# Kernel optimization log

Hardware: AMD Instinct MI355X
Metric: run time of the kernel (lower is better)

The kernel has to match this reference:

```python
import jax, jax.numpy as jnp
import numpy as np

N = 100000      # nodes
K = 16          # sampled neighbors per node (aggregate_num)
D = 256         # features_dim
DO = 256        # out_feat_dim
ALPHA = 0.2     # LeakyReLU negative slope (args.alpha)
EPS = 1e-12     # F.normalize eps


def setup_inputs() -> dict:
    key = jax.random.key(0)
    k1, k2, k3 = jax.random.split(key, 3)
    h = jax.random.normal(k1, (N, D), dtype=jnp.float32)
    neighbors = jax.random.randint(k2, (N, K), 0, N, dtype=jnp.int64)
    # Xavier-uniform-ish init for W_gcn
    limit = float(np.sqrt(6.0 / (D + DO)))
    W_gcn = jax.random.uniform(k3, (D, DO), dtype=jnp.float32, minval=-limit, maxval=limit)
    return {"h": h, "neighbors": neighbors, "W_gcn": W_gcn}


def reference(h, neighbors, W_gcn):
    # GCN-style aggregate: mean of self feature and K sampled neighbor features.
    # (dropout on neighbor feats is identity in eval mode)
    neigh_sum = jnp.sum(h[neighbors], axis=1)          # [N, D] gather + reduce
    agg = (h + neigh_sum) / jnp.float32(K + 1)         # [N, D]
    z = agg @ W_gcn                                    # [N, DO]
    z = jnp.where(z >= 0, z, ALPHA * z)                # LeakyReLU
    norm = jnp.sqrt(jnp.sum(z * z, axis=1, keepdims=True))
    return z / jnp.maximum(norm, EPS)                  # L2 normalize per row
```

## Files before the change

kernel.cpp:

```cpp
#include <hip/hip_runtime.h>
#include <stdint.h>

#define N_NODES 100000
#define KNBR 16
#define ALPHA 0.2f

typedef __attribute__((ext_vector_type(8))) short bf16x8;
typedef __attribute__((ext_vector_type(4))) float f32x4;
typedef __attribute__((ext_vector_type(4))) unsigned int u32x4;
typedef unsigned short u16;
typedef unsigned int u32;
typedef unsigned char u8;

static __device__ __forceinline__ u16 f2bf(float f) {
  u32 u = __builtin_bit_cast(u32, f);
  u += 0x7fffu + ((u >> 16) & 1u);
  return (u16)(u >> 16);
}

__global__ __launch_bounds__(256) void prep_w_kernel(const float* __restrict__ W,
                                                     u16* __restrict__ Wb) {
  const int t = blockIdx.x * 256 + threadIdx.x;
  const int l = t & 63;
  const int ct = (t >> 6) & 15;
  const int ks = t >> 10;
  const int colbase = ct * 16 + (l & 15);
  const int k0 = ks * 32 + (l >> 4) * 8;
  u32 wq[4];
#pragma unroll
  for (int q = 0; q < 4; ++q) {
    const u16 b0 = f2bf(W[(k0 + 2 * q) * 256 + colbase]);
    const u16 b1 = f2bf(W[(k0 + 2 * q + 1) * 256 + colbase]);
    wq[q] = (u32)b0 | ((u32)b1 << 16);
  }
  uint4 o = {wq[0], wq[1], wq[2], wq[3]};
  *(uint4*)(Wb + (size_t)t * 8) = o;
}

__global__ __launch_bounds__(256, 4) void gemm_kernel(const float* __restrict__ h,
                                                      const u16* __restrict__ Wb,
                                                      u8* __restrict__ Yq,
                                                      float* __restrict__ scale) {
  __shared__ __align__(16) u16 aS[32 * 256];
  __shared__ float redS[4][32];
  __shared__ float invSS[32];
  const int tid = threadIdx.x;
  const int blk = blockIdx.x;
  const size_t base = (size_t)blk * (32 * 256);

#pragma unroll
  for (int i = 0; i < 8; ++i) {
    const int flat = i * 1024 + tid * 4;
    const int row = flat >> 8, d0 = flat & 255;
    const f32x4 v = __builtin_nontemporal_load((const f32x4*)(h + base + flat));
    uint2 o;
    o.x = (u32)f2bf(v[0]) | ((u32)f2bf(v[1]) << 16);
    o.y = (u32)f2bf(v[2]) | ((u32)f2bf(v[3]) << 16);
    *(uint2*)((char*)aS + row * 512 + ((d0 * 2) ^ ((row & 7) << 4))) = o;
  }
  __syncthreads();

  const int l = tid & 63, wv = tid >> 6;
  const int l15 = l & 15, lg = l >> 4;
  f32x4 acc[2][4] = {};
  const uint4* wbL = ((const uint4*)Wb) + (size_t)(wv * 4) * 64 + l;
  const char* aggB = (const char*)aS;
  const int rb0 = l15 * 512;
  const int xm = (l15 & 7) << 4;
#pragma unroll 2
  for (int ks = 0; ks < 8; ++ks) {
    const int offk = ((ks * 64) + lg * 16) ^ xm;
    const bf16x8 a0 = *(const bf16x8*)(aggB + rb0 + offk);
    const bf16x8 a1 = *(const bf16x8*)(aggB + rb0 + 8192 + offk);
#pragma unroll
    for (int c = 0; c < 4; ++c) {
      const uint4 bw = wbL[ks * 1024 + c * 64];
      const bf16x8 b = __builtin_bit_cast(bf16x8, bw);
      acc[0][c] = __builtin_amdgcn_mfma_f32_16x16x32_bf16(a0, b, acc[0][c], 0, 0, 0);
      acc[1][c] = __builtin_amdgcn_mfma_f32_16x16x32_bf16(a1, b, acc[1][c], 0, 0, 0);
    }
  }

#pragma unroll
  for (int rt = 0; rt < 2; ++rt)
#pragma unroll
    for (int j = 0; j < 4; ++j) {
      float m = 0.f;
#pragma unroll
      for (int c = 0; c < 4; ++c) m = fmaxf(m, fabsf(acc[rt][c][j]));
      m = fmaxf(m, __shfl_xor(m, 1)); m = fmaxf(m, __shfl_xor(m, 2));
      m = fmaxf(m, __shfl_xor(m, 4)); m = fmaxf(m, __shfl_xor(m, 8));
      redS[wv][rt * 16 + lg * 4 + j] = m;
    }
  __syncthreads();
  if (tid < 32) {
    float m = fmaxf(fmaxf(redS[0][tid], redS[1][tid]),
                    fmaxf(redS[2][tid], redS[3][tid]));
    m = fmaxf(m, 1e-20f);
    scale[blk * 32 + tid] = m * (1.0f / 127.0f);
    invSS[tid] = 127.0f / m;
  }
  __syncthreads();

  u8* qS = (u8*)aS;
#pragma unroll
  for (int rt = 0; rt < 2; ++rt)
#pragma unroll
    for (int j = 0; j < 4; ++j) {
      const int r = rt * 16 + lg * 4 + j;
      const float inv = invSS[r];
      const int sw = ((r >> 2) & 7) << 5;
#pragma unroll
      for (int c = 0; c < 4; ++c) {
        float q = rintf(acc[rt][c][j] * inv);
        q = fminf(127.f, fmaxf(-127.f, q));
        qS[r * 256 + ((wv * 64 + c * 16 + l15) ^ sw)] = (u8)((int)q + 128);
      }
    }
  __syncthreads();

  const u32x4* q4 = (const u32x4*)aS;
  u32x4* yg = (u32x4*)(Yq + (size_t)blk * 8192);
#pragma unroll
  for (int q = 0; q < 2; ++q) {
    const int f = q * 4096 + tid * 16;
    const int row = f >> 8, col = f & 255;
    const int colx = col ^ (((row >> 2) & 7) << 5);
    __builtin_nontemporal_store(q4[(row * 256 + colx) >> 4], &yg[f >> 4]);
  }
}

__global__ __launch_bounds__(256) void gather_kernel(const u8* __restrict__ Yq,
                                                     const float* __restrict__ scale,
                                                     const int* __restrict__ nbr,
                                                     float* __restrict__ out) {
  const int tid = threadIdx.x;
  const int lane = tid & 63, wv = tid >> 6;
  const int node = __builtin_amdgcn_readfirstlane(blockIdx.x * 4 + wv);

  int idx[17];
  idx[0] = node;
#pragma unroll
  for (int j = 0; j < 16; ++j) idx[j + 1] = nbr[node * KNBR + j];

  float s[17];
#pragma unroll
  for (int j = 0; j < 17; ++j) s[j] = scale[idx[j]];

  u32 v[17];
#pragma unroll
  for (int j = 0; j < 17; ++j)
    v[j] = *(const u32*)(Yq + (size_t)idx[j] * 256 + lane * 4);

  float a0 = 0.f, a1 = 0.f, a2 = 0.f, a3 = 0.f, S = 0.f;
#pragma unroll
  for (int j = 0; j < 17; ++j) {
    float f0, f1, f2, f3;
    asm("v_cvt_f32_ubyte0 %0, %1" : "=v"(f0) : "v"(v[j]));
    asm("v_cvt_f32_ubyte1 %0, %1" : "=v"(f1) : "v"(v[j]));
    asm("v_cvt_f32_ubyte2 %0, %1" : "=v"(f2) : "v"(v[j]));
    asm("v_cvt_f32_ubyte3 %0, %1" : "=v"(f3) : "v"(v[j]));
    S += s[j];
    a0 = fmaf(s[j], f0, a0);
    a1 = fmaf(s[j], f1, a1);
    a2 = fmaf(s[j], f2, a2);
    a3 = fmaf(s[j], f3, a3);
  }
  const float sc = 1.0f / 17.0f, bias = 128.0f * S;
  a0 = (a0 - bias) * sc; a1 = (a1 - bias) * sc;
  a2 = (a2 - bias) * sc; a3 = (a3 - bias) * sc;
  a0 = (a0 >= 0.f) ? a0 : ALPHA * a0;
  a1 = (a1 >= 0.f) ? a1 : ALPHA * a1;
  a2 = (a2 >= 0.f) ? a2 : ALPHA * a2;
  a3 = (a3 >= 0.f) ? a3 : ALPHA * a3;

  float ss = a0 * a0 + a1 * a1 + a2 * a2 + a3 * a3;
  ss += __shfl_xor(ss, 1);  ss += __shfl_xor(ss, 2);
  ss += __shfl_xor(ss, 4);  ss += __shfl_xor(ss, 8);
  ss += __shfl_xor(ss, 16); ss += __shfl_xor(ss, 32);
  const float inv = 1.0f / fmaxf(sqrtf(ss), 1e-12f);

  f32x4 o = {a0 * inv, a1 * inv, a2 * inv, a3 * inv};
  __builtin_nontemporal_store(o, (f32x4*)(out + (size_t)node * 256 + lane * 4));
}

extern "C" void kernel_launch(void* const* d_in, const int* in_sizes, int n_in,
                              void* d_out, int out_size, void* d_ws, size_t ws_size,
                              hipStream_t stream) {
  const float* h = (const float*)d_in[0];
  const int* nbr = (const int*)d_in[1];
  const float* W = (const float*)d_in[2];
  float* out = (float*)d_out;

  u16* Wb = (u16*)d_ws;
  float* scale = (float*)((char*)d_ws + (1 << 17));
  u8* Yq = (u8*)((char*)d_ws + (1 << 20));

  prep_w_kernel<<<32, 256, 0, stream>>>(W, Wb);
  gemm_kernel<<<N_NODES / 32, 256, 0, stream>>>(h, Wb, Yq, scale);
  gather_kernel<<<N_NODES / 4, 256, 0, stream>>>(Yq, scale, nbr, out);
}
```

Baseline: 113.4 us.

## Slice quantized features by column for cache-local gather, add separate norm pass

The GEMM output is stored as eight column slices of 32 bytes per node, so each slice (3.2 MB) can stay cache-resident while a slice-gather kernel sums neighbor rows for that slice. The slice kernel writes partial bf16 results and per-slice sums of squares, and a new norm kernel reduces them and writes the normalized fp32 output. This trades extra global traffic (bf16 intermediate plus a third kernel launch) and bf16 rounding of the output for better locality of the random gathers. The fallback gather kernel also now loads the neighbor indices and scales once per wave and broadcasts them with readlane.

```diff
diff --git a/kernel.cpp b/kernel.cpp
--- a/kernel.cpp
+++ b/kernel.cpp
@@ -4,10 +4,14 @@
 #define N_NODES 100000
 #define KNBR 16
 #define ALPHA 0.2f
+#define SDIM 32
+#define NSLICE 8
+#define ANODES 64
 
 typedef __attribute__((ext_vector_type(8))) short bf16x8;
 typedef __attribute__((ext_vector_type(4))) float f32x4;
 typedef __attribute__((ext_vector_type(4))) unsigned int u32x4;
+typedef __attribute__((ext_vector_type(2))) unsigned int u32x2;
 typedef unsigned short u16;
 typedef unsigned int u32;
 typedef unsigned char u8;
@@ -16,6 +20,9 @@
   u32 u = __builtin_bit_cast(u32, f);
   u += 0x7fffu + ((u >> 16) & 1u);
   return (u16)(u >> 16);
+}
+static __device__ __forceinline__ float bf2f(u16 s) {
+  return __builtin_bit_cast(float, ((u32)s) << 16);
 }
 
 __global__ __launch_bounds__(256) void prep_w_kernel(const float* __restrict__ W,
@@ -37,6 +44,7 @@
   *(uint4*)(Wb + (size_t)t * 8) = o;
 }
 
+template <bool SLICED>
 __global__ __launch_bounds__(256, 4) void gemm_kernel(const float* __restrict__ h,
                                                       const u16* __restrict__ Wb,
                                                       u8* __restrict__ Yq,
@@ -120,14 +128,123 @@
   __syncthreads();
 
   const u32x4* q4 = (const u32x4*)aS;
-  u32x4* yg = (u32x4*)(Yq + (size_t)blk * 8192);
-#pragma unroll
-  for (int q = 0; q < 2; ++q) {
-    const int f = q * 4096 + tid * 16;
-    const int row = f >> 8, col = f & 255;
-    const int colx = col ^ (((row >> 2) & 7) << 5);
-    __builtin_nontemporal_store(q4[(row * 256 + colx) >> 4], &yg[f >> 4]);
-  }
+  if (SLICED) {
+#pragma unroll
+    for (int rr = 0; rr < 2; ++rr) {
+      const int f = rr * 256 + tid;
+      const int s = f >> 6;
+      const int nodeL = (f >> 1) & 31;
+      const int half = f & 1;
+      const int colx = (s * 32 + half * 16) ^ (((nodeL >> 2) & 7) << 5);
+      const u32x4 piece = q4[(nodeL * 256 + colx) >> 4];
+      __builtin_nontemporal_store(
+          piece, (u32x4*)(Yq + (size_t)s * ((size_t)N_NODES * SDIM) +
+                          (size_t)(blk * 32 + nodeL) * SDIM + half * 16));
+    }
+  } else {
+    u32x4* yg = (u32x4*)(Yq + (size_t)blk * 8192);
+#pragma unroll
+    for (int q = 0; q < 2; ++q) {
+      const int f = q * 4096 + tid * 16;
+      const int row = f >> 8, col = f & 255;
+      const int colx = col ^ (((row >> 2) & 7) << 5);
+      __builtin_nontemporal_store(q4[(row * 256 + colx) >> 4], &yg[f >> 4]);
+    }
+  }
+}
+
+__global__ __launch_bounds__(256) void slice_gather_kernel(
+    const u8* __restrict__ Yq, const float* __restrict__ scale,
+    const int* __restrict__ nbr, u16* __restrict__ zws,
+    float* __restrict__ ssp) {
+  __shared__ int nbrS[ANODES * 17];
+  const int tid = threadIdx.x;
+  const int s = blockIdx.x & 7;
+  const int chunk = blockIdx.x >> 3;
+  const int nodeBase = chunk * ANODES;
+
+  {
+    const int n = tid >> 2, j4 = tid & 3;
+    int4 v = {0, 0, 0, 0};
+    if (nodeBase + n < N_NODES)
+      v = ((const int4*)(nbr + (size_t)nodeBase * KNBR))[tid];
+    nbrS[n * 17 + j4 * 4 + 0] = v.x;
+    nbrS[n * 17 + j4 * 4 + 1] = v.y;
+    nbrS[n * 17 + j4 * 4 + 2] = v.z;
+    nbrS[n * 17 + j4 * 4 + 3] = v.w;
+  }
+  __syncthreads();
+
+  const u8* Ys = Yq + (size_t)s * ((size_t)N_NODES * SDIM);
+  const int sub = tid & 7;
+
+#pragma unroll
+  for (int p = 0; p < 2; ++p) {
+    const int nl = p * 32 + (tid >> 3);
+    const int node = nodeBase + nl;
+    if (node < N_NODES) {
+      int idx[17];
+      idx[0] = node;
+#pragma unroll
+      for (int j = 0; j < 16; ++j) idx[j + 1] = nbrS[nl * 17 + j];
+
+      u32 v[17];
+#pragma unroll
+      for (int j = 0; j < 17; ++j)
+        v[j] = *(const u32*)(Ys + (size_t)idx[j] * SDIM + sub * 4);
+      float sj[17];
+#pragma unroll
+      for (int j = 0; j < 17; ++j) sj[j] = scale[idx[j]];
+
+      float a0 = 0.f, a1 = 0.f, a2 = 0.f, a3 = 0.f, S = 0.f;
+#pragma unroll
+      for (int j = 0; j < 17; ++j) {
+        float f0, f1, f2, f3;
+        asm("v_cvt_f32_ubyte0 %0, %1" : "=v"(f0) : "v"(v[j]));
+        asm("v_cvt_f32_ubyte1 %0, %1" : "=v"(f1) : "v"(v[j]));
+        asm("v_cvt_f32_ubyte2 %0, %1" : "=v"(f2) : "v"(v[j]));
+        asm("v_cvt_f32_ubyte3 %0, %1" : "=v"(f3) : "v"(v[j]));
+        S += sj[j];
+        a0 = fmaf(sj[j], f0, a0);
+        a1 = fmaf(sj[j], f1, a1);
+        a2 = fmaf(sj[j], f2, a2);
+        a3 = fmaf(sj[j], f3, a3);
+      }
+      const float sc = 1.0f / 17.0f, bias = 128.0f * S;
+      a0 = (a0 - bias) * sc; a1 = (a1 - bias) * sc;
+      a2 = (a2 - bias) * sc; a3 = (a3 - bias) * sc;
+      a0 = (a0 >= 0.f) ? a0 : ALPHA * a0;
+      a1 = (a1 >= 0.f) ? a1 : ALPHA * a1;
+      a2 = (a2 >= 0.f) ? a2 : ALPHA * a2;
+      a3 = (a3 >= 0.f) ? a3 : ALPHA * a3;
+
+      float ss = a0 * a0 + a1 * a1 + a2 * a2 + a3 * a3;
+      ss += __shfl_xor(ss, 1); ss += __shfl_xor(ss, 2); ss += __shfl_xor(ss, 4);
+
+      u32x2 o = {(u32)f2bf(a0) | ((u32)f2bf(a1) << 16),
+                 (u32)f2bf(a2) | ((u32)f2bf(a3) << 16)};
+      __builtin_nontemporal_store(
+          o, (u32x2*)(zws + (size_t)node * 256 + s * SDIM + sub * 4));
+      if (sub == 0) ssp[node * 8 + s] = ss;
+    }
+  }
+}
+
+__global__ __launch_bounds__(256) void norm_kernel(const u16* __restrict__ zws,
+                                                   const float* __restrict__ ssp,
+                                                   float* __restrict__ out) {
+  const int tid = threadIdx.x;
+  const int lane = tid & 63, wv = tid >> 6;
+  const int node = __builtin_amdgcn_readfirstlane(blockIdx.x * 4 + wv);
+
+  float f = ssp[node * 8 + (lane & 7)];
+  f += __shfl_xor(f, 1); f += __shfl_xor(f, 2); f += __shfl_xor(f, 4);
+  const float inv = 1.0f / fmaxf(sqrtf(f), 1e-12f);
+
+  const u32x2 z = *(const u32x2*)(zws + (size_t)node * 256 + lane * 4);
+  f32x4 o = {bf2f((u16)(z.x & 0xffff)) * inv, bf2f((u16)(z.x >> 16)) * inv,
+             bf2f((u16)(z.y & 0xffff)) * inv, bf2f((u16)(z.y >> 16)) * inv};
+  __builtin_nontemporal_store(o, (f32x4*)(out + (size_t)node * 256 + lane * 4));
 }
 
 __global__ __launch_bounds__(256) void gather_kernel(const u8* __restrict__ Yq,
@@ -138,33 +255,40 @@
   const int lane = tid & 63, wv = tid >> 6;
   const int node = __builtin_amdgcn_readfirstlane(blockIdx.x * 4 + wv);
 
-  int idx[17];
-  idx[0] = node;
-#pragma unroll
-  for (int j = 0; j < 16; ++j) idx[j + 1] = nbr[node * KNBR + j];
-
-  float s[17];
-#pragma unroll
-  for (int j = 0; j < 17; ++j) s[j] = scale[idx[j]];
+  const int il = nbr[node * KNBR + (lane & 15)];
+  const float vscale = scale[il];
+  const float sself = scale[node];
+  const u32* yb = (const u32*)Yq;
 
   u32 v[17];
-#pragma unroll
-  for (int j = 0; j < 17; ++j)
-    v[j] = *(const u32*)(Yq + (size_t)idx[j] * 256 + lane * 4);
-
-  float a0 = 0.f, a1 = 0.f, a2 = 0.f, a3 = 0.f, S = 0.f;
-#pragma unroll
-  for (int j = 0; j < 17; ++j) {
+  v[0] = yb[(size_t)node * 64 + lane];
+#pragma unroll
+  for (int j = 0; j < 16; ++j) {
+    const int r = __builtin_amdgcn_readlane(il, j);
+    v[j + 1] = yb[(size_t)r * 64 + lane];
+  }
+
+  float a0, a1, a2, a3, S = sself;
+  {
     float f0, f1, f2, f3;
-    asm("v_cvt_f32_ubyte0 %0, %1" : "=v"(f0) : "v"(v[j]));
-    asm("v_cvt_f32_ubyte1 %0, %1" : "=v"(f1) : "v"(v[j]));
-    asm("v_cvt_f32_ubyte2 %0, %1" : "=v"(f2) : "v"(v[j]));
-    asm("v_cvt_f32_ubyte3 %0, %1" : "=v"(f3) : "v"(v[j]));
-    S += s[j];
-    a0 = fmaf(s[j], f0, a0);
-    a1 = fmaf(s[j], f1, a1);
-    a2 = fmaf(s[j], f2, a2);
-    a3 = fmaf(s[j], f3, a3);
+    asm("v_cvt_f32_ubyte0 %0, %1" : "=v"(f0) : "v"(v[0]));
+    asm("v_cvt_f32_ubyte1 %0, %1" : "=v"(f1) : "v"(v[0]));
+    asm("v_cvt_f32_ubyte2 %0, %1" : "=v"(f2) : "v"(v[0]));
+    asm("v_cvt_f32_ubyte3 %0, %1" : "=v"(f3) : "v"(v[0]));
+    a0 = sself * f0; a1 = sself * f1; a2 = sself * f2; a3 = sself * f3;
+  }
+#pragma unroll
+  for (int j = 0; j < 16; ++j) {
+    const float s = __builtin_bit_cast(
+        float, __builtin_amdgcn_readlane(__builtin_bit_cast(int, vscale), j));
+    float f0, f1, f2, f3;
+    asm("v_cvt_f32_ubyte0 %0, %1" : "=v"(f0) : "v"(v[j + 1]));
+    asm("v_cvt_f32_ubyte1 %0, %1" : "=v"(f1) : "v"(v[j + 1]));
+    asm("v_cvt_f32_ubyte2 %0, %1" : "=v"(f2) : "v"(v[j + 1]));
+    asm("v_cvt_f32_ubyte3 %0, %1" : "=v"(f3) : "v"(v[j + 1]));
+    S += s;
+    a0 = fmaf(s, f0, a0); a1 = fmaf(s, f1, a1);
+    a2 = fmaf(s, f2, a2); a3 = fmaf(s, f3, a3);
   }
   const float sc = 1.0f / 17.0f, bias = 128.0f * S;
   a0 = (a0 - bias) * sc; a1 = (a1 - bias) * sc;
@@ -192,11 +316,24 @@
   const float* W = (const float*)d_in[2];
   float* out = (float*)d_out;
 
-  u16* Wb = (u16*)d_ws;
-  float* scale = (float*)((char*)d_ws + (1 << 17));
-  u8* Yq = (u8*)((char*)d_ws + (1 << 20));
+  char* ws = (char*)d_ws;
+  u16* Wb = (u16*)ws;
+  float* scale = (float*)(ws + (1 << 17));
+  u8* Yq = (u8*)(ws + (1 << 20));
+  const size_t offZ = (1 << 20) + (size_t)N_NODES * 256;
+  u16* zws = (u16*)(ws + offZ);
+  const size_t offSsp = offZ + (size_t)N_NODES * 256 * 2;
+  float* ssp = (float*)(ws + offSsp);
+  const size_t need = offSsp + (size_t)N_NODES * 8 * 4;
 
   prep_w_kernel<<<32, 256, 0, stream>>>(W, Wb);
-  gemm_kernel<<<N_NODES / 32, 256, 0, stream>>>(h, Wb, Yq, scale);
-  gather_kernel<<<N_NODES / 4, 256, 0, stream>>>(Yq, scale, nbr, out);
-}
+  if (ws_size >= need) {
+    gemm_kernel<true><<<N_NODES / 32, 256, 0, stream>>>(h, Wb, Yq, scale);
+    const int chunks = (N_NODES + ANODES - 1) / ANODES;
+    slice_gather_kernel<<<chunks * 8, 256, 0, stream>>>(Yq, scale, nbr, zws, ssp);
+    norm_kernel<<<N_NODES / 4, 256, 0, stream>>>(zws, ssp, out);
+  } else {
+    gemm_kernel<false><<<N_NODES / 32, 256, 0, stream>>>(h, Wb, Yq, scale);
+    gather_kernel<<<N_NODES / 4, 256, 0, stream>>>(Yq, scale, nbr, out);
+  }
+}
```

New measurement: 190.3 us. 67.7% more time.

## Enlarge GEMM tile to 64 rows and gather 16B per lane with shared neighbor indices

Applied to the files above, without the earlier changes.

The GEMM kernel now handles 64 rows per block instead of 32, so each loaded weight fragment feeds four MFMA row tiles. This halves redundant W reads and block count, at the cost of more registers and LDS, hence lower occupancy. The gather kernel now processes 16 nodes per block, staging neighbor indices and scales in shared memory. Each lane loads 16 bytes per neighbor row instead of 4, cutting the number of memory requests, and the reduction shrinks to a 16-lane shuffle.

```diff
diff --git a/kernel.cpp b/kernel.cpp
--- a/kernel.cpp
+++ b/kernel.cpp
@@ -33,26 +33,28 @@
     const u16 b1 = f2bf(W[(k0 + 2 * q + 1) * 256 + colbase]);
     wq[q] = (u32)b0 | ((u32)b1 << 16);
   }
-  uint4 o = {wq[0], wq[1], wq[2], wq[3]};
-  *(uint4*)(Wb + (size_t)t * 8) = o;
-}
-
-__global__ __launch_bounds__(256, 4) void gemm_kernel(const float* __restrict__ h,
+  u32x4 o = {wq[0], wq[1], wq[2], wq[3]};
+  *(u32x4*)(Wb + (size_t)t * 8) = o;
+}
+
+__global__ __launch_bounds__(256, 3) void gemm_kernel(const float* __restrict__ h,
                                                       const u16* __restrict__ Wb,
                                                       u8* __restrict__ Yq,
                                                       float* __restrict__ scale) {
-  __shared__ __align__(16) u16 aS[32 * 256];
-  __shared__ float redS[4][32];
-  __shared__ float invSS[32];
+  __shared__ __align__(16) u16 aS[64 * 256];
+  __shared__ float redS[4][64];
+  __shared__ float invSS[64];
   const int tid = threadIdx.x;
   const int blk = blockIdx.x;
-  const size_t base = (size_t)blk * (32 * 256);
-
-#pragma unroll
-  for (int i = 0; i < 8; ++i) {
+  const size_t base = (size_t)blk * (64 * 256);
+
+#pragma unroll
+  for (int i = 0; i < 16; ++i) {
     const int flat = i * 1024 + tid * 4;
     const int row = flat >> 8, d0 = flat & 255;
-    const f32x4 v = __builtin_nontemporal_load((const f32x4*)(h + base + flat));
+    f32x4 v = {0.f, 0.f, 0.f, 0.f};
+    if (blk * 64 + row < N_NODES)
+      v = __builtin_nontemporal_load((const f32x4*)(h + base + flat));
     uint2 o;
     o.x = (u32)f2bf(v[0]) | ((u32)f2bf(v[1]) << 16);
     o.y = (u32)f2bf(v[2]) | ((u32)f2bf(v[3]) << 16);
@@ -62,27 +64,30 @@
 
   const int l = tid & 63, wv = tid >> 6;
   const int l15 = l & 15, lg = l >> 4;
-  f32x4 acc[2][4] = {};
-  const uint4* wbL = ((const uint4*)Wb) + (size_t)(wv * 4) * 64 + l;
+  f32x4 acc[4][4] = {};
+  const u32x4* wbL = ((const u32x4*)Wb) + (size_t)(wv * 4) * 64 + l;
   const char* aggB = (const char*)aS;
   const int rb0 = l15 * 512;
   const int xm = (l15 & 7) << 4;
 #pragma unroll 2
   for (int ks = 0; ks < 8; ++ks) {
     const int offk = ((ks * 64) + lg * 16) ^ xm;
-    const bf16x8 a0 = *(const bf16x8*)(aggB + rb0 + offk);
-    const bf16x8 a1 = *(const bf16x8*)(aggB + rb0 + 8192 + offk);
+    bf16x8 a[4];
+#pragma unroll
+    for (int rt = 0; rt < 4; ++rt)
+      a[rt] = *(const bf16x8*)(aggB + rt * 8192 + rb0 + offk);
 #pragma unroll
     for (int c = 0; c < 4; ++c) {
-      const uint4 bw = wbL[ks * 1024 + c * 64];
+      const u32x4 bw = wbL[ks * 1024 + c * 64];
       const bf16x8 b = __builtin_bit_cast(bf16x8, bw);
-      acc[0][c] = __builtin_amdgcn_mfma_f32_16x16x32_bf16(a0, b, acc[0][c], 0, 0, 0);
-      acc[1][c] = __builtin_amdgcn_mfma_f32_16x16x32_bf16(a1, b, acc[1][c], 0, 0, 0);
-    }
-  }
-
-#pragma unroll
-  for (int rt = 0; rt < 2; ++rt)
+#pragma unroll
+      for (int rt = 0; rt < 4; ++rt)
+        acc[rt][c] = __builtin_amdgcn_mfma_f32_16x16x32_bf16(a[rt], b, acc[rt][c], 0, 0, 0);
+    }
+  }
+
+#pragma unroll
+  for (int rt = 0; rt < 4; ++rt)
 #pragma unroll
     for (int j = 0; j < 4; ++j) {
       float m = 0.f;
@@ -93,18 +98,18 @@
       redS[wv][rt * 16 + lg * 4 + j] = m;
     }
   __syncthreads();
-  if (tid < 32) {
+  if (tid < 64) {
     float m = fmaxf(fmaxf(redS[0][tid], redS[1][tid]),
                     fmaxf(redS[2][tid], redS[3][tid]));
     m = fmaxf(m, 1e-20f);
-    scale[blk * 32 + tid] = m * (1.0f / 127.0f);
+    if (blk * 64 + tid < N_NODES) scale[blk * 64 + tid] = m * (1.0f / 127.0f);
     invSS[tid] = 127.0f / m;
   }
   __syncthreads();
 
   u8* qS = (u8*)aS;
 #pragma unroll
-  for (int rt = 0; rt < 2; ++rt)
+  for (int rt = 0; rt < 4; ++rt)
 #pragma unroll
     for (int j = 0; j < 4; ++j) {
       const int r = rt * 16 + lg * 4 + j;
@@ -120,68 +125,90 @@
   __syncthreads();
 
   const u32x4* q4 = (const u32x4*)aS;
-  u32x4* yg = (u32x4*)(Yq + (size_t)blk * 8192);
-#pragma unroll
-  for (int q = 0; q < 2; ++q) {
-    const int f = q * 4096 + tid * 16;
-    const int row = f >> 8, col = f & 255;
-    const int colx = col ^ (((row >> 2) & 7) << 5);
-    __builtin_nontemporal_store(q4[(row * 256 + colx) >> 4], &yg[f >> 4]);
-  }
-}
-
-__global__ __launch_bounds__(256) void gather_kernel(const u8* __restrict__ Yq,
-                                                     const float* __restrict__ scale,
-                                                     const int* __restrict__ nbr,
-                                                     float* __restrict__ out) {
+  u32x4* yg = (u32x4*)(Yq + (size_t)blk * 16384);
+#pragma unroll
+  for (int qq = 0; qq < 4; ++qq) {
+    const int f = qq * 256 + tid;
+    const int row = f >> 4;
+    const int colx = ((f & 15) * 16) ^ (((row >> 2) & 7) << 5);
+    if (blk * 64 + row < N_NODES)
+      __builtin_nontemporal_store(q4[(row * 256 + colx) >> 4], &yg[f]);
+  }
+}
+
+__global__ __launch_bounds__(256, 5) void gather_kernel(const u8* __restrict__ Yq,
+                                                        const float* __restrict__ scale,
+                                                        const int* __restrict__ nbr,
+                                                        float* __restrict__ out) {
+  __shared__ int nbrS[16][16];
+  __shared__ float sS[16][17];
   const int tid = threadIdx.x;
+  const int nb0 = blockIdx.x * 16;
+
+  {
+    const int n = tid >> 4, j = tid & 15;
+    const int idx = nbr[(nb0 + n) * KNBR + j];
+    nbrS[n][j] = idx;
+    sS[n][j] = scale[idx];
+    if (tid < 16) sS[tid][16] = scale[nb0 + tid];
+  }
+  __syncthreads();
+
   const int lane = tid & 63, wv = tid >> 6;
-  const int node = __builtin_amdgcn_readfirstlane(blockIdx.x * 4 + wv);
-
-  int idx[17];
-  idx[0] = node;
-#pragma unroll
-  for (int j = 0; j < 16; ++j) idx[j + 1] = nbr[node * KNBR + j];
-
-  float s[17];
-#pragma unroll
-  for (int j = 0; j < 17; ++j) s[j] = scale[idx[j]];
-
-  u32 v[17];
-#pragma unroll
-  for (int j = 0; j < 17; ++j)
-    v[j] = *(const u32*)(Yq + (size_t)idx[j] * 256 + lane * 4);
-
-  float a0 = 0.f, a1 = 0.f, a2 = 0.f, a3 = 0.f, S = 0.f;
+  const int qd = lane >> 4, l15 = lane & 15;
+  const int nl = wv * 4 + qd;
+  const int node = nb0 + nl;
+  const u32x4* yb = (const u32x4*)Yq;
+
+  u32x4 v[17];
+#pragma unroll
+  for (int j = 0; j < 16; ++j)
+    v[j] = yb[(size_t)nbrS[nl][j] * 16 + l15];
+  v[16] = yb[(size_t)node * 16 + l15];
+
+  float a[16];
+#pragma unroll
+  for (int k = 0; k < 16; ++k) a[k] = 0.f;
+  float S = 0.f;
 #pragma unroll
   for (int j = 0; j < 17; ++j) {
-    float f0, f1, f2, f3;
-    asm("v_cvt_f32_ubyte0 %0, %1" : "=v"(f0) : "v"(v[j]));
-    asm("v_cvt_f32_ubyte1 %0, %1" : "=v"(f1) : "v"(v[j]));
-    asm("v_cvt_f32_ubyte2 %0, %1" : "=v"(f2) : "v"(v[j]));
-    asm("v_cvt_f32_ubyte3 %0, %1" : "=v"(f3) : "v"(v[j]));
-    S += s[j];
-    a0 = fmaf(s[j], f0, a0);
-    a1 = fmaf(s[j], f1, a1);
-    a2 = fmaf(s[j], f2, a2);
-    a3 = fmaf(s[j], f3, a3);
-  }
+    const float sj = sS[nl][j];
+    S += sj;
+    const u32x4 w = v[j];
+#pragma unroll
+    for (int k = 0; k < 4; ++k) {
+      float f0, f1, f2, f3;
+      asm("v_cvt_f32_ubyte0 %0, %1" : "=v"(f0) : "v"(w[k]));
+      asm("v_cvt_f32_ubyte1 %0, %1" : "=v"(f1) : "v"(w[k]));
+      asm("v_cvt_f32_ubyte2 %0, %1" : "=v"(f2) : "v"(w[k]));
+      asm("v_cvt_f32_ubyte3 %0, %1" : "=v"(f3) : "v"(w[k]));
+      a[k * 4 + 0] = fmaf(sj, f0, a[k * 4 + 0]);
+      a[k * 4 + 1] = fmaf(sj, f1, a[k * 4 + 1]);
+      a[k * 4 + 2] = fmaf(sj, f2, a[k * 4 + 2]);
+      a[k * 4 + 3] = fmaf(sj, f3, a[k * 4 + 3]);
+    }
+  }
+
   const float sc = 1.0f / 17.0f, bias = 128.0f * S;
-  a0 = (a0 - bias) * sc; a1 = (a1 - bias) * sc;
-  a2 = (a2 - bias) * sc; a3 = (a3 - bias) * sc;
-  a0 = (a0 >= 0.f) ? a0 : ALPHA * a0;
-  a1 = (a1 >= 0.f) ? a1 : ALPHA * a1;
-  a2 = (a2 >= 0.f) ? a2 : ALPHA * a2;
-  a3 = (a3 >= 0.f) ? a3 : ALPHA * a3;
-
-  float ss = a0 * a0 + a1 * a1 + a2 * a2 + a3 * a3;
-  ss += __shfl_xor(ss, 1);  ss += __shfl_xor(ss, 2);
-  ss += __shfl_xor(ss, 4);  ss += __shfl_xor(ss, 8);
-  ss += __shfl_xor(ss, 16); ss += __shfl_xor(ss, 32);
+  float ss = 0.f;
+#pragma unroll
+  for (int k = 0; k < 16; ++k) {
+    float z = (a[k] - bias) * sc;
+    z = (z >= 0.f) ? z : ALPHA * z;
+    a[k] = z;
+    ss += z * z;
+  }
+  ss += __shfl_xor(ss, 1); ss += __shfl_xor(ss, 2);
+  ss += __shfl_xor(ss, 4); ss += __shfl_xor(ss, 8);
   const float inv = 1.0f / fmaxf(sqrtf(ss), 1e-12f);
 
-  f32x4 o = {a0 * inv, a1 * inv, a2 * inv, a3 * inv};
-  __builtin_nontemporal_store(o, (f32x4*)(out + (size_t)node * 256 + lane * 4));
+  float* op = out + (size_t)node * 256 + l15 * 16;
+#pragma unroll
+  for (int k = 0; k < 4; ++k) {
+    f32x4 o = {a[k * 4 + 0] * inv, a[k * 4 + 1] * inv,
+               a[k * 4 + 2] * inv, a[k * 4 + 3] * inv};
+    __builtin_nontemporal_store(o, (f32x4*)(op + k * 4));
+  }
 }
 
 extern "C" void kernel_launch(void* const* d_in, const int* in_sizes, int n_in,
@@ -192,11 +219,12 @@
   const float* W = (const float*)d_in[2];
   float* out = (float*)d_out;
 
-  u16* Wb = (u16*)d_ws;
-  float* scale = (float*)((char*)d_ws + (1 << 17));
-  u8* Yq = (u8*)((char*)d_ws + (1 << 20));
+  char* ws = (char*)d_ws;
+  u16* Wb = (u16*)ws;
+  float* scale = (float*)(ws + (1 << 17));
+  u8* Yq = (u8*)(ws + (1 << 20));
 
   prep_w_kernel<<<32, 256, 0, stream>>>(W, Wb);
-  gemm_kernel<<<N_NODES / 32, 256, 0, stream>>>(h, Wb, Yq, scale);
-  gather_kernel<<<N_NODES / 4, 256, 0, stream>>>(Yq, scale, nbr, out);
-}
+  gemm_kernel<<<(N_NODES + 63) / 64, 256, 0, stream>>>(h, Wb, Yq, scale);
+  gather_kernel<<<N_NODES / 16, 256, 0, stream>>>(Yq, scale, nbr, out);
+}
```

New measurement: 424.9 us. +274.6%, slower.
